# Optimization experiments

Hardware: AMD Instinct MI355X
Metric: run time of the kernel (lower is better)

Reference implementation:

```python
import jax, jax.numpy as jnp
import numpy as np

H = 512   # hidden_layer_neurons
E = 256   # char_embd_dim
S = 32    # source sequence length (encoder steps)
B = 1024  # batch_size
T = 32    # OUTPUT_MAX_LENGTH
V = 256   # target_len (vocab)
START = 1 # target_char_index['<']


def setup_inputs() -> dict:
    key = jax.random.key(0)
    ks = jax.random.split(key, 16)
    def rn(k, shape, scale=0.05):
        return jax.random.normal(k, shape, dtype=jnp.float32) * scale
    return {
        'decoder_current_state': rn(ks[0], (2, B, H), 1.0),
        'encoder_final_layers': rn(ks[1], (S, B, H), 1.0),
        'target_batch': jax.random.randint(ks[2], (B, T), 0, V, dtype=jnp.int32),
        'emb': rn(ks[3], (V, E)),
        'Wa': rn(ks[4], (H, H)), 'bWa': jnp.zeros((H,), jnp.float32),
        'Ua': rn(ks[5], (H, H)), 'bUa': jnp.zeros((H,), jnp.float32),
        'Va': rn(ks[6], (1, H)), 'bVa': jnp.zeros((1,), jnp.float32),
        'W_ih0': rn(ks[7], (3 * H, E + H)), 'W_hh0': rn(ks[8], (3 * H, H)),
        'b_ih0': jnp.zeros((3 * H,), jnp.float32), 'b_hh0': jnp.zeros((3 * H,), jnp.float32),
        'W_ih1': rn(ks[9], (3 * H, H)), 'W_hh1': rn(ks[10], (3 * H, H)),
        'b_ih1': jnp.zeros((3 * H,), jnp.float32), 'b_hh1': jnp.zeros((3 * H,), jnp.float32),
        'fcW': rn(ks[11], (V, H)), 'fcb': jnp.zeros((V,), jnp.float32),
    }


def _gru_cell(x, h, W_ih, W_hh, b_ih, b_hh):
    # PyTorch GRU cell math (gate order r, z, n)
    gi = x @ W_ih.T + b_ih
    gh = h @ W_hh.T + b_hh
    i_r, i_z, i_n = jnp.split(gi, 3, axis=-1)
    h_r, h_z, h_n = jnp.split(gh, 3, axis=-1)
    r = jax.nn.sigmoid(i_r + h_r)
    z = jax.nn.sigmoid(i_z + h_z)
    n = jnp.tanh(i_n + r * h_n)
    return (1.0 - z) * n + z * h


def _decode(decoder_current_state, encoder_final_layers, target_batch, emb,
            Wa, bWa, Ua, bUa, Va, bVa,
            W_ih0, W_hh0, b_ih0, b_hh0, W_ih1, W_hh1, b_ih1, b_hh1, fcW, fcb):
    # Ua(keys) is constant across decode steps -> hoist out of the scan.
    k_proj = jnp.einsum('sbh,gh->sbg', encoder_final_layers, Ua) + bUa  # (S,B,H)

    def step(carry, tgt_col):
        tok, state = carry                       # tok: (B,), state: (L,B,H)
        x = jax.nn.relu(emb[tok])                # (B,E)
        query = state[-1]                        # (B,H) top-layer hidden
        q_proj = query @ Wa.T + bWa              # (B,H)
        e = jnp.einsum('sbh,h->sb', jnp.tanh(q_proj[None] + k_proj), Va[0]) + bVa[0]
        w = jax.nn.softmax(e, axis=0)            # softmax over source dim (dim=0)
        context = jnp.einsum('sb,sbh->bh', w, encoder_final_layers)  # (B,H)
        gin = jnp.concatenate([x, context], axis=-1)                 # (B,E+H)
        h0 = _gru_cell(gin, state[0], W_ih0, W_hh0, b_ih0, b_hh0)
        h1 = _gru_cell(h0, state[1], W_ih1, W_hh1, b_ih1, b_hh1)
        new_state = jnp.stack([h0, h1])
        logp = jax.nn.log_softmax(h1 @ fcW.T + fcb, axis=-1)          # (B,V)
        next_tok = jnp.argmax(logp, axis=-1).astype(tok.dtype)        # greedy (detached topk)
        # NLLLoss(mean) against target_batch[:, i]
        step_loss = -jnp.take_along_axis(logp, tgt_col[:, None], axis=-1).mean()
        return (next_tok, new_state), (next_tok, w, step_loss)

    tok0 = jnp.full((target_batch.shape[0],), START, dtype=target_batch.dtype)
    (_, _), (toks, ws, losses) = jax.lax.scan(step, (tok0, decoder_current_state), target_batch.T)
    decoded = toks.T                                   # (B,T)
    attentions = jnp.transpose(ws, (0, 2, 1))[:, :, None, :]  # (T,B,1,S) like torch weights
    loss = losses.sum()
    correct = (decoded == target_batch).all(axis=1).sum()
    return decoded, attentions, loss, correct


def reference(decoder_current_state, encoder_final_layers, target_batch, emb,
              Wa, bWa, Ua, bUa, Va, bVa,
              W_ih0, W_hh0, b_ih0, b_hh0, W_ih1, W_hh1, b_ih1, b_hh1, fcW, fcb):
    return _decode(decoder_current_state, encoder_final_layers, target_batch, emb,
                   Wa, bWa, Ua, bUa, Va, bVa,
                   W_ih0, W_hh0, b_ih0, b_hh0, W_ih1, W_hh1, b_ih1, b_hh1, fcW, fcb)
```

## Files before the change

### kernel.cpp

```cpp
#include <hip/hip_runtime.h>
#include <math.h>

#define Hn 512
#define En 256
#define Sn 32
#define Bn 1024
#define Tn 32
#define Vn 256
#define G3 1536
#define EHn 768

__device__ __forceinline__ void fma4(float& acc, const float4 w, const float4 x) {
  acc = fmaf(w.x, x.x, acc);
  acc = fmaf(w.y, x.y, acc);
  acc = fmaf(w.z, x.z, acc);
  acc = fmaf(w.w, x.w, acc);
}

__global__ __launch_bounds__(256) void transpose_pack(const float* __restrict__ W,
                                                      float4* __restrict__ WT4,
                                                      int G, int K) {
  const int idx = blockIdx.x * blockDim.x + threadIdx.x;
  const int n = G * (K >> 2);
  if (idx >= n) return;
  const int k4 = idx / G, g = idx - k4 * G;
  WT4[idx] = *(const float4*)(W + (size_t)g * K + (k4 << 2));
}

__global__ __launch_bounds__(256) void gemm_bias(const float* __restrict__ A,
                                                 const float* __restrict__ Wt,
                                                 const float* __restrict__ bias,
                                                 float* __restrict__ C,
                                                 int M, int N, int K) {
  __shared__ float As[16][68];
  __shared__ float Ws[16][68];
  const int bm = blockIdx.y * 64;
  const int bn = blockIdx.x * 64;
  const int tid = threadIdx.x;
  const int tx = tid & 15;
  const int ty = tid >> 4;
  const int kk = tid & 15;
  const int r0 = tid >> 4;
  float acc[4][4] = {};
  for (int k0 = 0; k0 < K; k0 += 16) {
#pragma unroll
    for (int i = 0; i < 4; ++i) {
      const int m = r0 + (i << 4);
      As[kk][m] = A[(size_t)(bm + m) * K + (k0 + kk)];
      Ws[kk][m] = Wt[(size_t)(bn + m) * K + (k0 + kk)];
    }
    __syncthreads();
#pragma unroll
    for (int k = 0; k < 16; ++k) {
      const float4 a4 = *(const float4*)&As[k][ty * 4];
      const float4 w4 = *(const float4*)&Ws[k][tx * 4];
      const float av[4] = {a4.x, a4.y, a4.z, a4.w};
      const float wv[4] = {w4.x, w4.y, w4.z, w4.w};
#pragma unroll
      for (int i = 0; i < 4; ++i)
#pragma unroll
        for (int j = 0; j < 4; ++j) acc[i][j] = fmaf(av[i], wv[j], acc[i][j]);
    }
    __syncthreads();
  }
#pragma unroll
  for (int i = 0; i < 4; ++i) {
    const size_t m = (size_t)bm + ty * 4 + i;
    float* crow = C + m * N + bn + tx * 4;
#pragma unroll
    for (int j = 0; j < 4; ++j) crow[j] = acc[i][j] + bias[bn + tx * 4 + j];
  }
}


__global__ __launch_bounds__(1024) void attn_gin(
    const float* __restrict__ qp, const float* __restrict__ kproj,
    const float* __restrict__ enc, const float* __restrict__ emb,
    const int* __restrict__ tok, const float* __restrict__ Va,
    const float* __restrict__ bVa, float* __restrict__ gin,
    float* __restrict__ out, int t) {
  __shared__ __attribute__((aligned(16))) float qps[4 * Hn];
  __shared__ __attribute__((aligned(16))) float vas[Hn];
  __shared__ __attribute__((aligned(16))) float ep[1024];
  __shared__ float wrs[128];
  __shared__ int tokb[4];
  const int tid = threadIdx.x;
  const int b0 = blockIdx.x * 4;
  for (int i = tid; i < 4 * Hn; i += 1024)
    qps[i] = qp[(size_t)(b0 + (i >> 9)) * Hn + (i & 511)];
  if (tid < 512) vas[tid] = Va[tid];
  if (tid < 4) tokb[tid] = tok[b0 + tid];
  __syncthreads();
  {
    const int p = tid >> 3, q = tid & 7;
    const int r = p >> 5, s = p & 31;
    const float4* kp4 = (const float4*)(kproj + ((size_t)s * Bn + (b0 + r)) * Hn);
    const float4* qp4 = (const float4*)(qps + r * Hn);
    const float4* va4 = (const float4*)vas;
    float partial = 0.f;
    for (int i = 0; i < 16; i += 2) {
#pragma unroll
      for (int u = 0; u < 2; ++u) {
        const int f = q + ((i + u) << 3);
        const float4 k4 = kp4[f], q4 = qp4[f], v4 = va4[f];
        partial += v4.x * tanhf(q4.x + k4.x);
        partial += v4.y * tanhf(q4.y + k4.y);
        partial += v4.z * tanhf(q4.z + k4.z);
        partial += v4.w * tanhf(q4.w + k4.w);
      }
    }
    ep[tid] = partial;
  }
  __syncthreads();
  if (tid < 128) {
    float e = ep[tid * 8] + ep[tid * 8 + 1] + ep[tid * 8 + 2] + ep[tid * 8 + 3] +
              ep[tid * 8 + 4] + ep[tid * 8 + 5] + ep[tid * 8 + 6] + ep[tid * 8 + 7] +
              bVa[0];
    float m = e;
#pragma unroll
    for (int off = 16; off; off >>= 1) m = fmaxf(m, __shfl_xor(m, off));
    const float ex = expf(e - m);
    float ss = ex;
#pragma unroll
    for (int off = 16; off; off >>= 1) ss += __shfl_xor(ss, off);
    const float w = ex / ss;
    const int r = tid >> 5, s = tid & 31;
    wrs[tid] = w;
    out[(size_t)(Bn * Tn) + (size_t)t * (Bn * Sn) + (size_t)(b0 + r) * Sn + s] = w;
  }
  __syncthreads();
  {
    const int h = tid & 511, rp = tid >> 9;
    float c0 = 0.f, c1 = 0.f;
    const float* w0 = wrs + (2 * rp) * 32;
    const float* w1 = wrs + (2 * rp + 1) * 32;
#pragma unroll 4
    for (int s = 0; s < Sn; ++s) {
      const size_t base = ((size_t)s * Bn + b0 + 2 * rp) * Hn + h;
      c0 = fmaf(w0[s], enc[base], c0);
      c1 = fmaf(w1[s], enc[base + Hn], c1);
    }
    gin[(size_t)(b0 + 2 * rp) * EHn + En + h] = c0;
    gin[(size_t)(b0 + 2 * rp + 1) * EHn + En + h] = c1;
  }
  {
    const int r = tid >> 8, j = tid & 255;
    gin[(size_t)(b0 + r) * EHn + j] = fmaxf(emb[(size_t)tokb[r] * En + j], 0.f);
  }
}

template <int KIH4>
__global__ __launch_bounds__(512) void gru_gemm2(
    const float* __restrict__ xsrc, int xsF4,
    const float* __restrict__ hsrc,
    const float4* __restrict__ WihT, const float4* __restrict__ WhhT,
    const float* __restrict__ bih, const float* __restrict__ bhh,
    float* __restrict__ hdst) {
  __shared__ float4 xs4[64 * 16];
  __shared__ float4 ws4[16 * 3 * 32];
  const int tid = threadIdx.x;
  const int J0 = blockIdx.x * 32;
  const int R0 = blockIdx.y * 64;
  const int tx = tid & 31;
  const int ty = tid >> 5;
  const int row0 = ty * 4;
  float ar[4] = {}, az[4] = {}, ai[4] = {}, an[4] = {};
  const float4* x4 = (const float4*)xsrc;
  for (int c = 0; c < KIH4 / 16; ++c) {
    __syncthreads();
#pragma unroll
    for (int i = 0; i < 2; ++i) {
      const int idx = tid + i * 512;
      xs4[idx] = x4[(size_t)(R0 + (idx >> 4)) * xsF4 + c * 16 + (idx & 15)];
    }
#pragma unroll
    for (int i = 0; i < 3; ++i) {
      const int idx = tid + i * 512;
      const int k4 = idx / 96;
      const int rem = idx - k4 * 96;
      ws4[idx] = WihT[(size_t)(c * 16 + k4) * G3 + (rem >> 5) * 512 + J0 + (rem & 31)];
    }
    __syncthreads();
#pragma unroll 2
    for (int k4 = 0; k4 < 16; ++k4) {
      const float4 wr = ws4[(k4 * 3 + 0) * 32 + tx];
      const float4 wz = ws4[(k4 * 3 + 1) * 32 + tx];
      const float4 wn = ws4[(k4 * 3 + 2) * 32 + tx];
      float4 xr[4];
#pragma unroll
      for (int rr = 0; rr < 4; ++rr) xr[rr] = xs4[(row0 + rr) * 16 + k4];
#pragma unroll
      for (int rr = 0; rr < 4; ++rr) {
        fma4(ar[rr], wr, xr[rr]);
        fma4(az[rr], wz, xr[rr]);
        fma4(ai[rr], wn, xr[rr]);
      }
    }
  }
  const float4* h4 = (const float4*)hsrc;
  for (int c = 0; c < 8; ++c) {
    __syncthreads();
#pragma unroll
    for (int i = 0; i < 2; ++i) {
      const int idx = tid + i * 512;
      xs4[idx] = h4[(size_t)(R0 + (idx >> 4)) * (Hn / 4) + c * 16 + (idx & 15)];
    }
#pragma unroll
    for (int i = 0; i < 3; ++i) {
      const int idx = tid + i * 512;
      const int k4 = idx / 96;
      const int rem = idx - k4 * 96;
      ws4[idx] = WhhT[(size_t)(c * 16 + k4) * G3 + (rem >> 5) * 512 + J0 + (rem & 31)];
    }
    __syncthreads();
#pragma unroll 2
    for (int k4 = 0; k4 < 16; ++k4) {
      const float4 wr = ws4[(k4 * 3 + 0) * 32 + tx];
      const float4 wz = ws4[(k4 * 3 + 1) * 32 + tx];
      const float4 wn = ws4[(k4 * 3 + 2) * 32 + tx];
      float4 xr[4];
#pragma unroll
      for (int rr = 0; rr < 4; ++rr) xr[rr] = xs4[(row0 + rr) * 16 + k4];
#pragma unroll
      for (int rr = 0; rr < 4; ++rr) {
        fma4(ar[rr], wr, xr[rr]);
        fma4(az[rr], wz, xr[rr]);
        fma4(an[rr], wn, xr[rr]);
      }
    }
  }
  const int g0 = J0 + tx;
  const float bir = bih[g0], biz = bih[g0 + 512], bin = bih[g0 + 1024];
  const float bhr = bhh[g0], bhz = bhh[g0 + 512], bhn = bhh[g0 + 1024];
#pragma unroll
  for (int rr = 0; rr < 4; ++rr) {
    const int row = R0 + row0 + rr;
    const float rg = 1.f / (1.f + expf(-(ar[rr] + bir + bhr)));
    const float zg = 1.f / (1.f + expf(-(az[rr] + biz + bhz)));
    const float ng = tanhf(ai[rr] + bin + rg * (an[rr] + bhn));
    const float hold = hsrc[(size_t)row * Hn + g0];
    hdst[(size_t)row * Hn + g0] = (1.f - zg) * ng + zg * hold;
  }
}

__global__ __launch_bounds__(512) void fcqp_gemm(
    const float* __restrict__ h1,
    const float4* __restrict__ fcWT, const float* __restrict__ fcb,
    const float4* __restrict__ WaT, const float* __restrict__ bWa,
    float* __restrict__ logits, float* __restrict__ qp) {
  __shared__ float4 xs4[64 * 16];
  __shared__ float4 ws4[16 * 32];
  const int tid = threadIdx.x;
  const int jt = blockIdx.x;
  const int R0 = blockIdx.y * 64;
  const bool isfc = jt < 8;
  const int J0 = isfc ? jt * 32 : (jt - 8) * 32;
  const float4* W = isfc ? fcWT : WaT;
  const int ldW = isfc ? Vn : Hn;
  const int tx = tid & 31;
  const int ty = tid >> 5;
  const int row0 = ty * 4;
  float a[4] = {};
  const float4* h4 = (const float4*)h1;
  for (int c = 0; c < 8; ++c) {
    __syncthreads();
#pragma unroll
    for (int i = 0; i < 2; ++i) {
      const int idx = tid + i * 512;
      xs4[idx] = h4[(size_t)(R0 + (idx >> 4)) * (Hn / 4) + c * 16 + (idx & 15)];
    }
    ws4[tid] = W[(size_t)(c * 16 + (tid >> 5)) * ldW + J0 + (tid & 31)];
    __syncthreads();
#pragma unroll 4
    for (int k4 = 0; k4 < 16; ++k4) {
      const float4 w = ws4[k4 * 32 + tx];
      float4 xr[4];
#pragma unroll
      for (int rr = 0; rr < 4; ++rr) xr[rr] = xs4[(row0 + rr) * 16 + k4];
#pragma unroll
      for (int rr = 0; rr < 4; ++rr) fma4(a[rr], w, xr[rr]);
    }
  }
  if (isfc) {
    const float bb = fcb[J0 + tx];
#pragma unroll
    for (int rr = 0; rr < 4; ++rr)
      logits[(size_t)(R0 + row0 + rr) * Vn + J0 + tx] = a[rr] + bb;
  } else {
    const float bb = bWa[J0 + tx];
#pragma unroll
    for (int rr = 0; rr < 4; ++rr)
      qp[(size_t)(R0 + row0 + rr) * Hn + J0 + tx] = a[rr] + bb;
  }
}

__global__ __launch_bounds__(1024) void argmax_loss(
    const float* __restrict__ logits, const int* __restrict__ target, int t,
    int* __restrict__ tok, int* __restrict__ mf,
    float* __restrict__ out, float* __restrict__ wsloss) {
  __shared__ float wred[16];
  __shared__ int wredi[16];
  __shared__ float mxv[4], lgt[4];
  __shared__ int tgv[4];
  const int tid = threadIdx.x;
  const int b0 = blockIdx.x * 4;
  const int v = tid & 255, rr = tid >> 8;
  const float l = logits[(size_t)(b0 + rr) * Vn + v];
  if (tid < 4) tgv[tid] = target[(size_t)(b0 + tid) * Tn + t];
  __syncthreads();
  if (v == tgv[rr]) lgt[rr] = l;
  {
    float m = l;
    int mi = v;
#pragma unroll
    for (int off = 32; off; off >>= 1) {
      const float om = __shfl_xor(m, off);
      const int oi = __shfl_xor(mi, off);
      if (om > m || (om == m && oi < mi)) { m = om; mi = oi; }
    }
    if ((tid & 63) == 0) {
      wred[tid >> 6] = m;
      wredi[tid >> 6] = mi;
    }
  }
  __syncthreads();
  int am_r = 0;
  if (tid < 4) {
    float bm = wred[4 * tid];
    int bi = wredi[4 * tid];
#pragma unroll
    for (int q = 1; q < 4; ++q) {
      const float o = wred[4 * tid + q];
      const int oi = wredi[4 * tid + q];
      if (o > bm || (o == bm && oi < bi)) { bm = o; bi = oi; }
    }
    mxv[tid] = bm;
    am_r = bi;
  }
  __syncthreads();
  {
    float ex = expf(l - mxv[rr]);
#pragma unroll
    for (int off = 32; off; off >>= 1) ex += __shfl_xor(ex, off);
    if ((tid & 63) == 0) wred[tid >> 6] = ex;
  }
  __syncthreads();
  if (tid < 4) {
    tok[b0 + tid] = am_r;
    if (am_r != tgv[tid]) mf[b0 + tid] = 0;
    out[(size_t)(b0 + tid) * Tn + t] = (float)am_r;
  }
  if (tid == 0) {
    float lp = 0.f;
#pragma unroll
    for (int r = 0; r < 4; ++r) {
      const float s = wred[4 * r] + wred[4 * r + 1] + wred[4 * r + 2] + wred[4 * r + 3];
      lp += -(lgt[r] - mxv[r] - logf(s)) * (1.f / 1024.f);
    }
    atomicAdd(wsloss, lp);
  }
}

__global__ __launch_bounds__(1024) void qp_only(
    const float* __restrict__ h1src, const float4* __restrict__ WaT,
    const float* __restrict__ bWa, float* __restrict__ qp) {
  __shared__ __attribute__((aligned(16))) float h1s[4 * Hn];
  const int tid = threadIdx.x;
  const int b0 = blockIdx.x * 4;
  for (int i = tid; i < 4 * Hn; i += 1024)
    h1s[i] = h1src[(size_t)(b0 + (i >> 9)) * Hn + (i & 511)];
  __syncthreads();
  const int jj = (tid & 31) | ((tid >> 6) << 5);
  const int grp = (tid >> 5) & 1;
  const int k0 = grp * 64;
  const float4* wp = WaT + jj + (size_t)k0 * Hn;
  float a0 = 0.f, a1 = 0.f, a2 = 0.f, a3 = 0.f;
  for (int k4 = 0; k4 < 64; k4 += 2) {
#pragma unroll
    for (int u = 0; u < 2; ++u) {
      const float4 w = wp[(size_t)(k4 + u) * Hn];
      const float4 x0 = ((const float4*)(h1s))[k0 + k4 + u];
      const float4 x1 = ((const float4*)(h1s + Hn))[k0 + k4 + u];
      const float4 x2 = ((const float4*)(h1s + 2 * Hn))[k0 + k4 + u];
      const float4 x3 = ((const float4*)(h1s + 3 * Hn))[k0 + k4 + u];
      fma4(a0, w, x0); fma4(a1, w, x1); fma4(a2, w, x2); fma4(a3, w, x3);
    }
  }
  a0 += __shfl_xor(a0, 32);
  a1 += __shfl_xor(a1, 32);
  a2 += __shfl_xor(a2, 32);
  a3 += __shfl_xor(a3, 32);
  const float bb = bWa[jj];
  if (!grp) {
    qp[(size_t)(b0 + 0) * Hn + jj] = a0 + bb;
    qp[(size_t)(b0 + 1) * Hn + jj] = a1 + bb;
  } else {
    qp[(size_t)(b0 + 2) * Hn + jj] = a2 + bb;
    qp[(size_t)(b0 + 3) * Hn + jj] = a3 + bb;
  }
}

__global__ void init_bufs(int* tok, int* mf, float* wsloss) {
  const int i = blockIdx.x * blockDim.x + threadIdx.x;
  if (i < Bn) { tok[i] = 1; mf[i] = 1; }
  if (i == 0) wsloss[0] = 0.f;
}

__global__ __launch_bounds__(1024) void finisher2(const float* __restrict__ wsloss,
                                                  const int* __restrict__ mf,
                                                  float* __restrict__ out) {
  __shared__ int s[1024];
  const int tid = threadIdx.x;
  s[tid] = mf[tid];
  __syncthreads();
  for (int off = 512; off; off >>= 1) {
    if (tid < off) s[tid] += s[tid + off];
    __syncthreads();
  }
  if (tid == 0) {
    const size_t base = (size_t)Bn * Tn + (size_t)Tn * Bn * Sn;
    out[base] = wsloss[0];
    out[base + 1] = (float)s[0];
  }
}

template <int KCI, int KCH>
__device__ __forceinline__ void gru_pair(
    int jj, int grp,
    const float4* __restrict__ WihT,
    const float4* __restrict__ WhhT,
    const float* __restrict__ x, int xstride,
    float* __restrict__ h,
    const float* __restrict__ bih, const float* __restrict__ bhh) {
  float ar[4] = {}, az[4] = {}, ain[4] = {}, ahn[4] = {};
  {
    const int k0 = grp * KCI;
    const float4* w0 = WihT + jj + (size_t)k0 * G3;
    const float4* w1 = WihT + jj + 512 + (size_t)k0 * G3;
    const float4* w2 = WihT + jj + 1024 + (size_t)k0 * G3;
    for (int k4 = 0; k4 < KCI; k4 += 2) {
#pragma unroll
      for (int u = 0; u < 2; ++u) {
        const float4 a = w0[(size_t)(k4 + u) * G3];
        const float4 b = w1[(size_t)(k4 + u) * G3];
        const float4 c = w2[(size_t)(k4 + u) * G3];
#pragma unroll
        for (int r = 0; r < 4; ++r) {
          const float4 xv = ((const float4*)(x + r * xstride))[k0 + k4 + u];
          fma4(ar[r], a, xv);
          fma4(az[r], b, xv);
          fma4(ain[r], c, xv);
        }
      }
    }
  }
  {
    const int k0 = grp * KCH;
    const float4* w0 = WhhT + jj + (size_t)k0 * G3;
    const float4* w1 = WhhT + jj + 512 + (size_t)k0 * G3;
    const float4* w2 = WhhT + jj + 1024 + (size_t)k0 * G3;
    for (int k4 = 0; k4 < KCH; k4 += 2) {
#pragma unroll
      for (int u = 0; u < 2; ++u) {
        const float4 a = w0[(size_t)(k4 + u) * G3];
        const float4 b = w1[(size_t)(k4 + u) * G3];
        const float4 c = w2[(size_t)(k4 + u) * G3];
#pragma unroll
        for (int r = 0; r < 4; ++r) {
          const float4 xv = ((const float4*)(h + r * Hn))[k0 + k4 + u];
          fma4(ar[r], a, xv);
          fma4(az[r], b, xv);
          fma4(ahn[r], c, xv);
        }
      }
    }
  }
#pragma unroll
  for (int r = 0; r < 4; ++r) {
    ar[r] += __shfl_xor(ar[r], 32);
    az[r] += __shfl_xor(az[r], 32);
    ain[r] += __shfl_xor(ain[r], 32);
    ahn[r] += __shfl_xor(ahn[r], 32);
  }
  const float bir = bih[jj], biz = bih[jj + 512], bin = bih[jj + 1024];
  const float bhr = bhh[jj], bhz = bhh[jj + 512], bhn = bhh[jj + 1024];
  const int r2 = grp * 2;
  const float s0r = (grp ? ar[2] : ar[0]) + bir + bhr;
  const float s0z = (grp ? az[2] : az[0]) + biz + bhz;
  const float s0i = (grp ? ain[2] : ain[0]) + bin;
  const float s0h = (grp ? ahn[2] : ahn[0]) + bhn;
  const float s1r = (grp ? ar[3] : ar[1]) + bir + bhr;
  const float s1z = (grp ? az[3] : az[1]) + biz + bhz;
  const float s1i = (grp ? ain[3] : ain[1]) + bin;
  const float s1h = (grp ? ahn[3] : ahn[1]) + bhn;
  const float rg0 = 1.f / (1.f + expf(-s0r));
  const float zg0 = 1.f / (1.f + expf(-s0z));
  const float ng0 = tanhf(s0i + rg0 * s0h);
  const float rg1 = 1.f / (1.f + expf(-s1r));
  const float zg1 = 1.f / (1.f + expf(-s1z));
  const float ng1 = tanhf(s1i + rg1 * s1h);
  const float h0old = h[(r2 + 0) * Hn + jj];
  const float h1old = h[(r2 + 1) * Hn + jj];
  const float hn0 = (1.f - zg0) * ng0 + zg0 * h0old;
  const float hn1 = (1.f - zg1) * ng1 + zg1 * h1old;
  __syncthreads();
  h[(r2 + 0) * Hn + jj] = hn0;
  h[(r2 + 1) * Hn + jj] = hn1;
  __syncthreads();
}

__global__ __launch_bounds__(1024) __attribute__((amdgpu_waves_per_eu(4, 4)))
void decoder_r4y(
    const float* __restrict__ state, const float* __restrict__ enc,
    const int* __restrict__ target, const float* __restrict__ emb,
    const float4* __restrict__ WaT, const float* __restrict__ bWa,
    const float* __restrict__ Va, const float* __restrict__ bVa,
    const float4* __restrict__ W0ihT, const float4* __restrict__ W0hhT,
    const float* __restrict__ bih0, const float* __restrict__ bhh0,
    const float4* __restrict__ W1ihT, const float4* __restrict__ W1hhT,
    const float* __restrict__ bih1, const float* __restrict__ bhh1,
    const float4* __restrict__ fcWT, const float* __restrict__ fcb,
    const float* __restrict__ kproj, float* __restrict__ out,
    float* __restrict__ wsloss, int* __restrict__ wscorrect) {
  __shared__ __attribute__((aligned(16))) float h0s[4 * Hn];
  __shared__ __attribute__((aligned(16))) float h1s[4 * Hn];
  __shared__ __attribute__((aligned(16))) float qps[4 * Hn];
  __shared__ __attribute__((aligned(16))) float gins[4 * EHn];
  __shared__ __attribute__((aligned(16))) float vas[Hn];
  __shared__ __attribute__((aligned(16))) float wrs[4 * Sn];
  __shared__ __attribute__((aligned(16))) float ep[1024];
  __shared__ float wred[16];
  __shared__ int wredi[16];
  __shared__ float mxv[4], lgt[4];
  __shared__ int tgv[4], tokb[4], mfs[4];

  const int tid = threadIdx.x;
  const int b0 = blockIdx.x * 4;
  const int jj = (tid & 31) | ((tid >> 6) << 5);
  const int grp = (tid >> 5) & 1;

  for (int i = tid; i < 4 * Hn; i += 1024) {
    const int r = i >> 9, j = i & 511;
    h0s[i] = state[(size_t)(b0 + r) * Hn + j];
    h1s[i] = state[(size_t)(Bn + b0 + r) * Hn + j];
  }
  if (tid < 512) vas[tid] = Va[tid];
  if (tid < 4) { tokb[tid] = 1; mfs[tid] = 1; }
  __syncthreads();

  float run_loss = 0.f;

  for (int t = 0; t < Tn; ++t) {
    {
      const int kc = (Hn >> 2) >> 1;
      const int k0 = grp * kc;
      const float4* wp = WaT + jj + (size_t)k0 * Hn;
      float a0 = 0.f, a1 = 0.f, a2 = 0.f, a3 = 0.f;
      for (int k4 = 0; k4 < 64; k4 += 2) {
#pragma unroll
        for (int u = 0; u < 2; ++u) {
          const float4 w = wp[(size_t)(k4 + u) * Hn];
          const float4 x0 = ((const float4*)(h1s))[k0 + k4 + u];
          const float4 x1 = ((const float4*)(h1s + Hn))[k0 + k4 + u];
          const float4 x2 = ((const float4*)(h1s + 2 * Hn))[k0 + k4 + u];
          const float4 x3 = ((const float4*)(h1s + 3 * Hn))[k0 + k4 + u];
          fma4(a0, w, x0); fma4(a1, w, x1); fma4(a2, w, x2); fma4(a3, w, x3);
        }
      }
      a0 += __shfl_xor(a0, 32);
      a1 += __shfl_xor(a1, 32);
      a2 += __shfl_xor(a2, 32);
      a3 += __shfl_xor(a3, 32);
      const float bb = bWa[jj];
      if (!grp) {
        qps[jj] = a0 + bb;
        qps[Hn + jj] = a1 + bb;
      } else {
        qps[2 * Hn + jj] = a2 + bb;
        qps[3 * Hn + jj] = a3 + bb;
      }
    }
    __syncthreads();
    {
      const int p = tid >> 3, q = tid & 7;
      const int r = p >> 5, s = p & 31;
      const float4* kp4 = (const float4*)(kproj + ((size_t)s * Bn + (b0 + r)) * Hn);
      const float4* qp4 = (const float4*)(qps + r * Hn);
      const float4* va4 = (const float4*)vas;
      float partial = 0.f;
      for (int i = 0; i < 16; i += 2) {
#pragma unroll
        for (int u = 0; u < 2; ++u) {
          const int f = q + ((i + u) << 3);
          const float4 k4 = kp4[f], q4 = qp4[f], v4 = va4[f];
          partial += v4.x * tanhf(q4.x + k4.x);
          partial += v4.y * tanhf(q4.y + k4.y);
          partial += v4.z * tanhf(q4.z + k4.z);
          partial += v4.w * tanhf(q4.w + k4.w);
        }
      }
      ep[tid] = partial;
    }
    __syncthreads();
    if (tid < 128) {
      float e = ep[tid * 8] + ep[tid * 8 + 1] + ep[tid * 8 + 2] + ep[tid * 8 + 3] +
                ep[tid * 8 + 4] + ep[tid * 8 + 5] + ep[tid * 8 + 6] + ep[tid * 8 + 7] +
                bVa[0];
      float m = e;
#pragma unroll
      for (int off = 16; off; off >>= 1) m = fmaxf(m, __shfl_xor(m, off));
      const float ex = expf(e - m);
      float ss = ex;
#pragma unroll
      for (int off = 16; off; off >>= 1) ss += __shfl_xor(ss, off);
      const float w = ex / ss;
      const int r = tid >> 5, s = tid & 31;
      wrs[tid] = w;
      out[(size_t)(Bn * Tn) + (size_t)t * (Bn * Sn) + (size_t)(b0 + r) * Sn + s] = w;
    }
    __syncthreads();
    {
      const int h = tid & 511, rp = tid >> 9;
      float c0 = 0.f, c1 = 0.f;
      const float* w0 = wrs + (2 * rp) * 32;
      const float* w1 = wrs + (2 * rp + 1) * 32;
#pragma unroll 4
      for (int s = 0; s < Sn; ++s) {
        const size_t base = ((size_t)s * Bn + b0 + 2 * rp) * Hn + h;
        c0 = fmaf(w0[s], enc[base], c0);
        c1 = fmaf(w1[s], enc[base + Hn], c1);
      }
      gins[(2 * rp) * EHn + En + h] = c0;
      gins[(2 * rp + 1) * EHn + En + h] = c1;
    }
    {
      const int r = tid >> 8, j = tid & 255;
      gins[r * EHn + j] = fmaxf(emb[(size_t)tokb[r] * En + j], 0.f);
    }
    if (tid < 4) tgv[tid] = target[(size_t)(b0 + tid) * Tn + t];
    __syncthreads();
    gru_pair<96, 64>(jj, grp, W0ihT, W0hhT, gins, EHn, h0s, bih0, bhh0);
    gru_pair<64, 64>(jj, grp, W1ihT, W1hhT, h0s, Hn, h1s, bih1, bhh1);
    const int v = tid & 255, rr = tid >> 8;
    float l;
    {
      const float4* wp = fcWT + v;
      const float4* xr = (const float4*)(h1s + rr * Hn);
      float acc = 0.f;
      for (int k4 = 0; k4 < (Hn >> 2); k4 += 4) {
#pragma unroll
        for (int u = 0; u < 4; ++u) {
          const float4 w = wp[(size_t)(k4 + u) * Vn];
          fma4(acc, w, xr[k4 + u]);
        }
      }
      l = acc + fcb[v];
    }
    if (v == tgv[rr]) lgt[rr] = l;
    {
      float m = l;
      int mi = v;
#pragma unroll
      for (int off = 32; off; off >>= 1) {
        const float om = __shfl_xor(m, off);
        const int oi = __shfl_xor(mi, off);
        if (om > m || (om == m && oi < mi)) { m = om; mi = oi; }
      }
      if ((tid & 63) == 0) {
        wred[tid >> 6] = m;
        wredi[tid >> 6] = mi;
      }
    }
    __syncthreads();
    int am_r = 0;
    if (tid < 4) {
      float bm = wred[4 * tid];
      int bi = wredi[4 * tid];
#pragma unroll
      for (int q = 1; q < 4; ++q) {
        const float o = wred[4 * tid + q];
        const int oi = wredi[4 * tid + q];
        if (o > bm || (o == bm && oi < bi)) { bm = o; bi = oi; }
      }
      mxv[tid] = bm;
      am_r = bi;
    }
    __syncthreads();
    {
      float ex = expf(l - mxv[rr]);
#pragma unroll
      for (int off = 32; off; off >>= 1) ex += __shfl_xor(ex, off);
      if ((tid & 63) == 0) wred[tid >> 6] = ex;
    }
    __syncthreads();
    if (tid < 4) {
      tokb[tid] = am_r;
      if (am_r != tgv[tid]) mfs[tid] = 0;
      out[(size_t)(b0 + tid) * Tn + t] = (float)am_r;
    }
    if (tid == 0) {
#pragma unroll
      for (int r = 0; r < 4; ++r) {
        const float s = wred[4 * r] + wred[4 * r + 1] + wred[4 * r + 2] + wred[4 * r + 3];
        run_loss += -(lgt[r] - mxv[r] - logf(s)) * (1.f / 1024.f);
      }
    }
  }

  __syncthreads();
  if (tid == 0) {
    atomicAdd(wsloss, run_loss);
    atomicAdd(wscorrect, mfs[0] + mfs[1] + mfs[2] + mfs[3]);
  }
}

__global__ void ws_init(float* wsloss, int* wscorrect) {
  wsloss[0] = 0.f;
  wscorrect[0] = 0;
}

__global__ void finisher(const float* __restrict__ wsloss,
                         const int* __restrict__ wscorrect, float* __restrict__ out) {
  const size_t base = (size_t)Bn * Tn + (size_t)Tn * Bn * Sn;
  out[base] = wsloss[0];
  out[base + 1] = (float)wscorrect[0];
}

extern "C" void kernel_launch(void* const* d_in, const int* in_sizes, int n_in,
                              void* d_out, int out_size, void* d_ws, size_t ws_size,
                              hipStream_t stream) {
  const float* state = (const float*)d_in[0];
  const float* enc = (const float*)d_in[1];
  const int* target = (const int*)d_in[2];
  const float* emb = (const float*)d_in[3];
  const float* Wa = (const float*)d_in[4];
  const float* bWa = (const float*)d_in[5];
  const float* Ua = (const float*)d_in[6];
  const float* bUa = (const float*)d_in[7];
  const float* Va = (const float*)d_in[8];
  const float* bVa = (const float*)d_in[9];
  const float* Wih0 = (const float*)d_in[10];
  const float* Whh0 = (const float*)d_in[11];
  const float* bih0 = (const float*)d_in[12];
  const float* bhh0 = (const float*)d_in[13];
  const float* Wih1 = (const float*)d_in[14];
  const float* Whh1 = (const float*)d_in[15];
  const float* bih1 = (const float*)d_in[16];
  const float* bhh1 = (const float*)d_in[17];
  const float* fcW = (const float*)d_in[18];
  const float* fcb = (const float*)d_in[19];
  float* out = (float*)d_out;

  const size_t KPROJ_FLOATS = (size_t)Sn * Bn * Hn;

  const size_t N0IH = (size_t)G3 * (EHn / 4);
  const size_t NHH = (size_t)G3 * (Hn / 4);
  const size_t NWA = (size_t)Hn * (Hn / 4);
  const size_t NFC = (size_t)Vn * (Hn / 4);
  const size_t WT_TOTAL = N0IH + 3 * NHH + NWA + NFC;
  const size_t NEED_A2 = WT_TOTAL * 16 + KPROJ_FLOATS * 4 + 256;

  const size_t NGIN = (size_t)Bn * EHn;
  const size_t NH = (size_t)Bn * Hn;
  const size_t NLG = (size_t)Bn * Vn;
  const size_t EXTRA = NGIN + 5 * NH + NLG;
  const size_t NEED_NEW = NEED_A2 + EXTRA * 4 + 4 * 2048 + 256;

  if (ws_size >= NEED_NEW) {
    float4* W0ihT = (float4*)d_ws;
    float4* W0hhT = W0ihT + N0IH;
    float4* W1ihT = W0hhT + NHH;
    float4* W1hhT = W1ihT + NHH;
    float4* WaT = W1hhT + NHH;
    float4* fcWT = WaT + NWA;
    float* kproj = (float*)(fcWT + NFC);
    float* gin = kproj + KPROJ_FLOATS;
    float* h0A = gin + NGIN;
    float* h0B = h0A + NH;
    float* h1A = h0B + NH;
    float* h1B = h1A + NH;
    float* qpbuf = h1B + NH;
    float* logits = qpbuf + NH;
    int* tok = (int*)(logits + NLG);
    int* mf = tok + Bn;
    float* wsloss = (float*)(mf + Bn);

    init_bufs<<<2, 512, 0, stream>>>(tok, mf, wsloss);
    transpose_pack<<<(int)((N0IH + 255) / 256), 256, 0, stream>>>(Wih0, W0ihT, G3, EHn);
    transpose_pack<<<(int)((NHH + 255) / 256), 256, 0, stream>>>(Whh0, W0hhT, G3, Hn);
    transpose_pack<<<(int)((NHH + 255) / 256), 256, 0, stream>>>(Wih1, W1ihT, G3, Hn);
    transpose_pack<<<(int)((NHH + 255) / 256), 256, 0, stream>>>(Whh1, W1hhT, G3, Hn);
    transpose_pack<<<(int)((NWA + 255) / 256), 256, 0, stream>>>(Wa, WaT, Hn, Hn);
    transpose_pack<<<(int)((NFC + 255) / 256), 256, 0, stream>>>(fcW, fcWT, Vn, Hn);
    gemm_bias<<<dim3(Hn / 64, (Sn * Bn) / 64), 256, 0, stream>>>(
        enc, Ua, bUa, kproj, Sn * Bn, Hn, Hn);
    qp_only<<<Bn / 4, 1024, 0, stream>>>(state + (size_t)Bn * Hn, WaT, bWa, qpbuf);

    for (int t = 0; t < Tn; ++t) {
      const float* h0cur = (t == 0) ? state : ((t & 1) ? h0A : h0B);
      float* h0nxt = (t & 1) ? h0B : h0A;
      const float* h1cur =
          (t == 0) ? (state + (size_t)Bn * Hn) : ((t & 1) ? h1A : h1B);
      float* h1nxt = (t & 1) ? h1B : h1A;

      attn_gin<<<Bn / 4, 1024, 0, stream>>>(qpbuf, kproj, enc, emb, tok, Va, bVa,
                                            gin, out, t);
      gru_gemm2<192><<<dim3(16, 16), 512, 0, stream>>>(
          gin, EHn / 4, h0cur, W0ihT, W0hhT, bih0, bhh0, h0nxt);
      gru_gemm2<128><<<dim3(16, 16), 512, 0, stream>>>(
          h0nxt, Hn / 4, h1cur, W1ihT, W1hhT, bih1, bhh1, h1nxt);
      fcqp_gemm<<<dim3(24, 16), 512, 0, stream>>>(h1nxt, fcWT, fcb, WaT, bWa,
                                                  logits, qpbuf);
      argmax_loss<<<Bn / 4, 1024, 0, stream>>>(logits, target, t, tok, mf, out,
                                               wsloss);
    }
    finisher2<<<1, 1024, 0, stream>>>(wsloss, mf, out);
  } else if (ws_size >= NEED_A2) {
    float4* W0ihT = (float4*)d_ws;
    float4* W0hhT = W0ihT + N0IH;
    float4* W1ihT = W0hhT + NHH;
    float4* W1hhT = W1ihT + NHH;
    float4* WaT = W1hhT + NHH;
    float4* fcWT = WaT + NWA;
    float* kproj = (float*)(fcWT + NFC);
    float* wsloss = kproj + KPROJ_FLOATS;
    int* wscorrect = (int*)(wsloss + 1);

    ws_init<<<1, 1, 0, stream>>>(wsloss, wscorrect);
    transpose_pack<<<(int)((N0IH + 255) / 256), 256, 0, stream>>>(Wih0, W0ihT, G3, EHn);
    transpose_pack<<<(int)((NHH + 255) / 256), 256, 0, stream>>>(Whh0, W0hhT, G3, Hn);
    transpose_pack<<<(int)((NHH + 255) / 256), 256, 0, stream>>>(Wih1, W1ihT, G3, Hn);
    transpose_pack<<<(int)((NHH + 255) / 256), 256, 0, stream>>>(Whh1, W1hhT, G3, Hn);
    transpose_pack<<<(int)((NWA + 255) / 256), 256, 0, stream>>>(Wa, WaT, Hn, Hn);
    transpose_pack<<<(int)((NFC + 255) / 256), 256, 0, stream>>>(fcW, fcWT, Vn, Hn);
    gemm_bias<<<dim3(Hn / 64, (Sn * Bn) / 64), 256, 0, stream>>>(
        enc, Ua, bUa, kproj, Sn * Bn, Hn, Hn);
    decoder_r4y<<<Bn / 4, 1024, 0, stream>>>(
        state, enc, target, emb, WaT, bWa, Va, bVa, W0ihT, W0hhT, bih0, bhh0,
        W1ihT, W1hhT, bih1, bhh1, fcWT, fcb, kproj, out, wsloss, wscorrect);
    finisher<<<1, 1, 0, stream>>>(wsloss, wscorrect, out);
  }
}
```

Before: 7.809 ms.

## Fuse argmax/loss into attention kernel and register-prefetch GEMM tiles

The per-step argmax and NLL loss reduction is folded into the start of the next step's attention kernel, which reads the previous logits directly. Only the final step keeps a standalone argmax launch, so one kernel launch per decode step is removed. The GRU and fc/qp GEMMs now prefetch the next K-chunk into registers while the current chunk is computed, merging the input and hidden loops into a single pipelined loop, and they request two waves per EU. The trade-off is more register pressure and extra reduction work and barriers inside the attention kernel.

```diff
diff --git a/kernel.cpp b/kernel.cpp
--- a/kernel.cpp
+++ b/kernel.cpp
@@ -74,22 +74,86 @@
 
 
 __global__ __launch_bounds__(1024) void attn_gin(
+    const float* __restrict__ logits, const int* __restrict__ target,
+    int t, int use_am,
     const float* __restrict__ qp, const float* __restrict__ kproj,
     const float* __restrict__ enc, const float* __restrict__ emb,
-    const int* __restrict__ tok, const float* __restrict__ Va,
-    const float* __restrict__ bVa, float* __restrict__ gin,
-    float* __restrict__ out, int t) {
+    const float* __restrict__ Va, const float* __restrict__ bVa,
+    float* __restrict__ gin, int* __restrict__ mf,
+    float* __restrict__ out, float* __restrict__ wsloss) {
   __shared__ __attribute__((aligned(16))) float qps[4 * Hn];
   __shared__ __attribute__((aligned(16))) float vas[Hn];
   __shared__ __attribute__((aligned(16))) float ep[1024];
   __shared__ float wrs[128];
-  __shared__ int tokb[4];
+  __shared__ float wred[16];
+  __shared__ int wredi[16];
+  __shared__ float mxv[4], lgt[4];
+  __shared__ int tgv[4], tokb[4];
   const int tid = threadIdx.x;
   const int b0 = blockIdx.x * 4;
+  const int v = tid & 255, rr = tid >> 8;
+
   for (int i = tid; i < 4 * Hn; i += 1024)
     qps[i] = qp[(size_t)(b0 + (i >> 9)) * Hn + (i & 511)];
   if (tid < 512) vas[tid] = Va[tid];
-  if (tid < 4) tokb[tid] = tok[b0 + tid];
+  float l = 0.f;
+  if (use_am) {
+    l = logits[(size_t)(b0 + rr) * Vn + v];
+    if (tid < 4) tgv[tid] = target[(size_t)(b0 + tid) * Tn + (t - 1)];
+  } else {
+    if (tid < 4) tokb[tid] = 1;
+  }
+  __syncthreads();
+  if (use_am) {
+    if (v == tgv[rr]) lgt[rr] = l;
+    {
+      float m = l;
+      int mi = v;
+#pragma unroll
+      for (int off = 32; off; off >>= 1) {
+        const float om = __shfl_xor(m, off);
+        const int oi = __shfl_xor(mi, off);
+        if (om > m || (om == m && oi < mi)) { m = om; mi = oi; }
+      }
+      if ((tid & 63) == 0) {
+        wred[tid >> 6] = m;
+        wredi[tid >> 6] = mi;
+      }
+    }
+    __syncthreads();
+    if (tid < 4) {
+      float bm = wred[4 * tid];
+      int bi = wredi[4 * tid];
+#pragma unroll
+      for (int q = 1; q < 4; ++q) {
+        const float o = wred[4 * tid + q];
+        const int oi = wredi[4 * tid + q];
+        if (o > bm || (o == bm && oi < bi)) { bm = o; bi = oi; }
+      }
+      mxv[tid] = bm;
+      tokb[tid] = bi;
+      if (bi != tgv[tid]) mf[b0 + tid] = 0;
+      out[(size_t)(b0 + tid) * Tn + (t - 1)] = (float)bi;
+    }
+    __syncthreads();
+    {
+      float ex = expf(l - mxv[rr]);
+#pragma unroll
+      for (int off = 32; off; off >>= 1) ex += __shfl_xor(ex, off);
+      if ((tid & 63) == 0) wred[tid >> 6] = ex;
+    }
+    __syncthreads();
+    if (tid == 0) {
+      float lp = 0.f;
+#pragma unroll
+      for (int r = 0; r < 4; ++r) {
+        const float s =
+            wred[4 * r] + wred[4 * r + 1] + wred[4 * r + 2] + wred[4 * r + 3];
+        lp += -(lgt[r] - mxv[r] - logf(s)) * (1.f / 1024.f);
+      }
+      atomicAdd(wsloss, lp);
+    }
+  }
   __syncthreads();
   {
     const int p = tid >> 3, q = tid & 7;
@@ -149,8 +213,29 @@
   }
 }
 
+__device__ __forceinline__ void gru_chunk(
+    const float4* __restrict__ xs4, const float4* __restrict__ ws4,
+    int row0, int tx, float (&ar)[4], float (&az)[4], float (&aw)[4]) {
+#pragma unroll 2
+  for (int k4 = 0; k4 < 16; ++k4) {
+    const float4 wr = ws4[(k4 * 3 + 0) * 32 + tx];
+    const float4 wz = ws4[(k4 * 3 + 1) * 32 + tx];
+    const float4 wn = ws4[(k4 * 3 + 2) * 32 + tx];
+    float4 xr[4];
+#pragma unroll
+    for (int rr = 0; rr < 4; ++rr) xr[rr] = xs4[(row0 + rr) * 16 + k4];
+#pragma unroll
+    for (int rr = 0; rr < 4; ++rr) {
+      fma4(ar[rr], wr, xr[rr]);
+      fma4(az[rr], wz, xr[rr]);
+      fma4(aw[rr], wn, xr[rr]);
+    }
+  }
+}
+
 template <int KIH4>
-__global__ __launch_bounds__(512) void gru_gemm2(
+__global__ __launch_bounds__(512) __attribute__((amdgpu_waves_per_eu(2)))
+void gru_gemm3(
     const float* __restrict__ xsrc, int xsF4,
     const float* __restrict__ hsrc,
     const float4* __restrict__ WihT, const float4* __restrict__ WhhT,
@@ -164,70 +249,50 @@
   const int tx = tid & 31;
   const int ty = tid >> 5;
   const int row0 = ty * 4;
+  constexpr int NCI = KIH4 / 16;
+  const int xr0 = tid >> 4, xf0 = tid & 15;
+  const int xr1 = (tid + 512) >> 4, xf1 = (tid + 512) & 15;
+  const int wk0 = tid / 96, wm0 = tid - wk0 * 96;
+  const int wk1 = (tid + 512) / 96, wm1 = (tid + 512) - wk1 * 96;
+  const int wk2 = (tid + 1024) / 96, wm2 = (tid + 1024) - wk2 * 96;
+  const int wo0 = (wm0 >> 5) * 512 + J0 + (wm0 & 31);
+  const int wo1 = (wm1 >> 5) * 512 + J0 + (wm1 & 31);
+  const int wo2 = (wm2 >> 5) * 512 + J0 + (wm2 & 31);
+  const float4* x4 = (const float4*)xsrc;
+  const float4* h4 = (const float4*)hsrc;
   float ar[4] = {}, az[4] = {}, ai[4] = {}, an[4] = {};
-  const float4* x4 = (const float4*)xsrc;
-  for (int c = 0; c < KIH4 / 16; ++c) {
-    __syncthreads();
-#pragma unroll
-    for (int i = 0; i < 2; ++i) {
-      const int idx = tid + i * 512;
-      xs4[idx] = x4[(size_t)(R0 + (idx >> 4)) * xsF4 + c * 16 + (idx & 15)];
-    }
-#pragma unroll
-    for (int i = 0; i < 3; ++i) {
-      const int idx = tid + i * 512;
-      const int k4 = idx / 96;
-      const int rem = idx - k4 * 96;
-      ws4[idx] = WihT[(size_t)(c * 16 + k4) * G3 + (rem >> 5) * 512 + J0 + (rem & 31)];
-    }
-    __syncthreads();
-#pragma unroll 2
-    for (int k4 = 0; k4 < 16; ++k4) {
-      const float4 wr = ws4[(k4 * 3 + 0) * 32 + tx];
-      const float4 wz = ws4[(k4 * 3 + 1) * 32 + tx];
-      const float4 wn = ws4[(k4 * 3 + 2) * 32 + tx];
-      float4 xr[4];
-#pragma unroll
-      for (int rr = 0; rr < 4; ++rr) xr[rr] = xs4[(row0 + rr) * 16 + k4];
-#pragma unroll
-      for (int rr = 0; rr < 4; ++rr) {
-        fma4(ar[rr], wr, xr[rr]);
-        fma4(az[rr], wz, xr[rr]);
-        fma4(ai[rr], wn, xr[rr]);
-      }
-    }
-  }
-  const float4* h4 = (const float4*)hsrc;
-  for (int c = 0; c < 8; ++c) {
-    __syncthreads();
-#pragma unroll
-    for (int i = 0; i < 2; ++i) {
-      const int idx = tid + i * 512;
-      xs4[idx] = h4[(size_t)(R0 + (idx >> 4)) * (Hn / 4) + c * 16 + (idx & 15)];
-    }
-#pragma unroll
-    for (int i = 0; i < 3; ++i) {
-      const int idx = tid + i * 512;
-      const int k4 = idx / 96;
-      const int rem = idx - k4 * 96;
-      ws4[idx] = WhhT[(size_t)(c * 16 + k4) * G3 + (rem >> 5) * 512 + J0 + (rem & 31)];
-    }
-    __syncthreads();
-#pragma unroll 2
-    for (int k4 = 0; k4 < 16; ++k4) {
-      const float4 wr = ws4[(k4 * 3 + 0) * 32 + tx];
-      const float4 wz = ws4[(k4 * 3 + 1) * 32 + tx];
-      const float4 wn = ws4[(k4 * 3 + 2) * 32 + tx];
-      float4 xr[4];
-#pragma unroll
-      for (int rr = 0; rr < 4; ++rr) xr[rr] = xs4[(row0 + rr) * 16 + k4];
-#pragma unroll
-      for (int rr = 0; rr < 4; ++rr) {
-        fma4(ar[rr], wr, xr[rr]);
-        fma4(az[rr], wz, xr[rr]);
-        fma4(an[rr], wn, xr[rr]);
-      }
-    }
+  float4 px0 = x4[(size_t)(R0 + xr0) * xsF4 + xf0];
+  float4 px1 = x4[(size_t)(R0 + xr1) * xsF4 + xf1];
+  float4 pw0 = WihT[(size_t)wk0 * G3 + wo0];
+  float4 pw1 = WihT[(size_t)wk1 * G3 + wo1];
+  float4 pw2 = WihT[(size_t)wk2 * G3 + wo2];
+  for (int c = 0; c < NCI + 8; ++c) {
+    __syncthreads();
+    xs4[tid] = px0;
+    xs4[tid + 512] = px1;
+    ws4[tid] = pw0;
+    ws4[tid + 512] = pw1;
+    ws4[tid + 1024] = pw2;
+    if (c + 1 < NCI) {
+      const int cc = c + 1;
+      px0 = x4[(size_t)(R0 + xr0) * xsF4 + cc * 16 + xf0];
+      px1 = x4[(size_t)(R0 + xr1) * xsF4 + cc * 16 + xf1];
+      pw0 = WihT[(size_t)(cc * 16 + wk0) * G3 + wo0];
+      pw1 = WihT[(size_t)(cc * 16 + wk1) * G3 + wo1];
+      pw2 = WihT[(size_t)(cc * 16 + wk2) * G3 + wo2];
+    } else if (c + 1 < NCI + 8) {
+      const int cc = c + 1 - NCI;
+      px0 = h4[(size_t)(R0 + xr0) * (Hn / 4) + cc * 16 + xf0];
+      px1 = h4[(size_t)(R0 + xr1) * (Hn / 4) + cc * 16 + xf1];
+      pw0 = WhhT[(size_t)(cc * 16 + wk0) * G3 + wo0];
+      pw1 = WhhT[(size_t)(cc * 16 + wk1) * G3 + wo1];
+      pw2 = WhhT[(size_t)(cc * 16 + wk2) * G3 + wo2];
+    }
+    __syncthreads();
+    if (c < NCI)
+      gru_chunk(xs4, ws4, row0, tx, ar, az, ai);
+    else
+      gru_chunk(xs4, ws4, row0, tx, ar, az, an);
   }
   const int g0 = J0 + tx;
   const float bir = bih[g0], biz = bih[g0 + 512], bin = bih[g0 + 1024];
@@ -243,7 +308,8 @@
   }
 }
 
-__global__ __launch_bounds__(512) void fcqp_gemm(
+__global__ __launch_bounds__(512) __attribute__((amdgpu_waves_per_eu(2)))
+void fcqp_gemm(
     const float* __restrict__ h1,
     const float4* __restrict__ fcWT, const float* __restrict__ fcb,
     const float4* __restrict__ WaT, const float* __restrict__ bWa,
@@ -260,16 +326,25 @@
   const int tx = tid & 31;
   const int ty = tid >> 5;
   const int row0 = ty * 4;
+  const int xr0 = tid >> 4, xf0 = tid & 15;
+  const int xr1 = (tid + 512) >> 4, xf1 = (tid + 512) & 15;
+  const int wk = tid >> 5, wc = tid & 31;
   float a[4] = {};
   const float4* h4 = (const float4*)h1;
+  float4 px0 = h4[(size_t)(R0 + xr0) * (Hn / 4) + xf0];
+  float4 px1 = h4[(size_t)(R0 + xr1) * (Hn / 4) + xf1];
+  float4 pw = W[(size_t)wk * ldW + J0 + wc];
   for (int c = 0; c < 8; ++c) {
     __syncthreads();
-#pragma unroll
-    for (int i = 0; i < 2; ++i) {
-      const int idx = tid + i * 512;
-      xs4[idx] = h4[(size_t)(R0 + (idx >> 4)) * (Hn / 4) + c * 16 + (idx & 15)];
-    }
-    ws4[tid] = W[(size_t)(c * 16 + (tid >> 5)) * ldW + J0 + (tid & 31)];
+    xs4[tid] = px0;
+    xs4[tid + 512] = px1;
+    ws4[tid] = pw;
+    if (c + 1 < 8) {
+      const int cc = c + 1;
+      px0 = h4[(size_t)(R0 + xr0) * (Hn / 4) + cc * 16 + xf0];
+      px1 = h4[(size_t)(R0 + xr1) * (Hn / 4) + cc * 16 + xf1];
+      pw = W[(size_t)(cc * 16 + wk) * ldW + J0 + wc];
+    }
     __syncthreads();
 #pragma unroll 4
     for (int k4 = 0; k4 < 16; ++k4) {
@@ -803,17 +878,18 @@
           (t == 0) ? (state + (size_t)Bn * Hn) : ((t & 1) ? h1A : h1B);
       float* h1nxt = (t & 1) ? h1B : h1A;
 
-      attn_gin<<<Bn / 4, 1024, 0, stream>>>(qpbuf, kproj, enc, emb, tok, Va, bVa,
-                                            gin, out, t);
-      gru_gemm2<192><<<dim3(16, 16), 512, 0, stream>>>(
+      attn_gin<<<Bn / 4, 1024, 0, stream>>>(logits, target, t, (t > 0) ? 1 : 0,
+                                            qpbuf, kproj, enc, emb, Va, bVa,
+                                            gin, mf, out, wsloss);
+      gru_gemm3<192><<<dim3(16, 16), 512, 0, stream>>>(
           gin, EHn / 4, h0cur, W0ihT, W0hhT, bih0, bhh0, h0nxt);
-      gru_gemm2<128><<<dim3(16, 16), 512, 0, stream>>>(
+      gru_gemm3<128><<<dim3(16, 16), 512, 0, stream>>>(
           h0nxt, Hn / 4, h1cur, W1ihT, W1hhT, bih1, bhh1, h1nxt);
       fcqp_gemm<<<dim3(24, 16), 512, 0, stream>>>(h1nxt, fcWT, fcb, WaT, bWa,
                                                   logits, qpbuf);
-      argmax_loss<<<Bn / 4, 1024, 0, stream>>>(logits, target, t, tok, mf, out,
-                                               wsloss);
-    }
+    }
+    argmax_loss<<<Bn / 4, 1024, 0, stream>>>(logits, target, Tn - 1, tok, mf, out,
+                                             wsloss);
     finisher2<<<1, 1024, 0, stream>>>(wsloss, mf, out);
   } else if (ws_size >= NEED_A2) {
     float4* W0ihT = (float4*)d_ws;
```

Result: faster. 7.640 ms (-2.2%).
